# Kernel tuning notes

Hardware: AMD Instinct MI355X
Metric: run time of the kernel (lower is better)

## Reference

```python
import jax, jax.numpy as jnp
import numpy as np

KH, KW, STRIDE, PAD = 3, 3, 1, 1
TREE_DEPTH = 3
NUM_LEAVES = 2 ** TREE_DEPTH  # 8
NUM_NODES = NUM_LEAVES - 1    # 7
OUT_CH, IN_CH = 256, 64
B, H, W = 16, 48, 48
PATCH_LEN = IN_CH * KH * KW   # 576

# Each of the 16 relaxed binary logic gates g_k(a,b) is affine in (1, a, b, a*b):
#   g_k(a,b) = c0 + c1*a + c2*b + c3*(a*b)
# Rows follow the standard difflogic gate ordering (gate 3 = pass-through a).
GATE_COEFF = np.array([
    [0.,  0.,  0.,  0.],   # 0: FALSE
    [0.,  0.,  0.,  1.],   # 1: a AND b
    [0.,  1.,  0., -1.],   # 2: a AND NOT b
    [0.,  1.,  0.,  0.],   # 3: a
    [0.,  0.,  1., -1.],   # 4: NOT a AND b
    [0.,  0.,  1.,  0.],   # 5: b
    [0.,  1.,  1., -2.],   # 6: a XOR b
    [0.,  1.,  1., -1.],   # 7: a OR b
    [1., -1., -1.,  1.],   # 8: NOT (a OR b)
    [1., -1., -1.,  2.],   # 9: NOT (a XOR b)
    [1.,  0., -1.,  0.],   # 10: NOT b
    [1.,  0., -1.,  1.],   # 11: a OR NOT b
    [1., -1.,  0.,  0.],   # 12: NOT a
    [1., -1.,  0.,  1.],   # 13: NOT a OR b
    [1.,  0.,  0., -1.],   # 14: NOT (a AND b)
    [1.,  0.,  0.,  0.],   # 15: TRUE
], dtype=np.float32)


def _unfold(x):
    # x: (B, C, Hp, Wp) -> (B, C*KH*KW, Ho*Wo), channel-major then row-major
    # kernel ordering (matches torch.nn.functional.unfold).
    b, c, hp, wp = x.shape
    ho = (hp - KH) // STRIDE + 1
    wo = (wp - KW) // STRIDE + 1
    cols = jnp.stack(
        [x[:, :, i:i + STRIDE * ho:STRIDE, j:j + STRIDE * wo:STRIDE]
         for i in range(KH) for j in range(KW)], axis=2)  # (B, C, KH*KW, Ho, Wo)
    return cols.reshape(b, c * KH * KW, ho * wo), ho, wo


def setup_inputs() -> dict:
    key = jax.random.key(0)
    k1, k2, k3 = jax.random.split(key, 3)
    x = jax.random.uniform(k1, (B, IN_CH, H, W), dtype=jnp.float32)
    logits = jax.random.normal(k2, (OUT_CH, NUM_NODES, 16), dtype=jnp.float32)
    leaf_indices = jax.random.randint(k3, (OUT_CH, NUM_LEAVES), 0, PATCH_LEN, dtype=jnp.int32)
    return {"x": x, "logits": logits, "leaf_indices": leaf_indices}


def reference(x, logits, leaf_indices):
    b = x.shape[0]
    o = logits.shape[0]
    xp = jnp.pad(x, ((0, 0), (0, 0), (PAD, PAD), (PAD, PAD)))
    patches, ho, wo = _unfold(xp)          # (B, patch_len, L)
    cur = patches[:, leaf_indices, :]      # gather leaves: (B, O, num_leaves, L)
    coeff = jnp.asarray(GATE_COEFF)        # (16, 4)
    node_ptr = 0
    width = NUM_LEAVES
    for _ in range(TREE_DEPTH):
        nc = width // 2
        a = cur[:, :, 0::2, :]             # (B, O, nc, L)
        bb = cur[:, :, 1::2, :]
        probs = jax.nn.softmax(logits[:, node_ptr:node_ptr + nc, :], axis=-1)  # (O, nc, 16)
        # softmax-weighted mixture of the 16 gates = affine combo in (1, a, b, ab)
        w = jnp.einsum('ong,gc->onc', probs, coeff)  # (O, nc, 4)
        w = w[None, :, :, :, None]                   # (1, O, nc, 4, 1)
        cur = w[:, :, :, 0] + w[:, :, :, 1] * a + w[:, :, :, 2] * bb + w[:, :, :, 3] * (a * bb)
        node_ptr += nc
        width = nc
    y = cur[:, :, 0, :]                    # (B, O, L)
    return y.reshape(b, o, ho, wo)
```

## Files before the change

### kernel.cpp

```cpp
#include <hip/hip_runtime.h>

#define NB 16
#define IN_CH 64
#define OUT_CH 256
#define NH 48
#define NW 48
#define NPIX (NH * NW)
#define ROW_STRIDE 52
#define CH_STRIDE (4 * ROW_STRIDE)
#define LDS_DW (IN_CH * CH_STRIDE)
#define NITEMS (IN_CH * 4 * 26)
#define META_F4 9

__constant__ float c_gate[16 * 4] = {
    0.f, 0.f, 0.f, 0.f,
    0.f, 0.f, 0.f, 1.f,
    0.f, 1.f, 0.f, -1.f,
    0.f, 1.f, 0.f, 0.f,
    0.f, 0.f, 1.f, -1.f,
    0.f, 0.f, 1.f, 0.f,
    0.f, 1.f, 1.f, -2.f,
    0.f, 1.f, 1.f, -1.f,
    1.f, -1.f, -1.f, 1.f,
    1.f, -1.f, -1.f, 2.f,
    1.f, 0.f, -1.f, 0.f,
    1.f, 0.f, -1.f, 1.f,
    1.f, -1.f, 0.f, 0.f,
    1.f, -1.f, 0.f, 1.f,
    1.f, 0.f, 0.f, -1.f,
    1.f, 0.f, 0.f, 0.f
};

__global__ __launch_bounds__(256) void prep_kernel(
    const float* __restrict__ logits,
    const int*   __restrict__ leaf_idx,
    float*       __restrict__ meta)
{
    int t = blockIdx.x * 256 + threadIdx.x;
    if (t < OUT_CH * 8) {
        int idx = leaf_idx[t];
        int c  = idx / 9;
        int k  = idx - c * 9;
        int di = k / 3;
        int dj = k - di * 3;
        reinterpret_cast<int*>(meta)[(t >> 3) * 36 + (t & 7)] =
            c * CH_STRIDE + di * ROW_STRIDE + dj;
    } else {
        int t2 = t - OUT_CH * 8;
        if (t2 >= OUT_CH * 7) return;
        int o = t2 / 7;
        int n = t2 - o * 7;
        const float* lg = logits + (size_t)t2 * 16;

        float m = lg[0];
#pragma unroll
        for (int g = 1; g < 16; ++g) m = fmaxf(m, lg[g]);
        float e16[16];
        float s = 0.f;
#pragma unroll
        for (int g = 0; g < 16; ++g) { e16[g] = expf(lg[g] - m); s += e16[g]; }
        float inv = 1.f / s;

        float w0 = 0.f, w1 = 0.f, w2 = 0.f, w3 = 0.f;
#pragma unroll
        for (int g = 0; g < 16; ++g) {
            float p = e16[g] * inv;
            w0 += p * c_gate[g * 4 + 0];
            w1 += p * c_gate[g * 4 + 1];
            w2 += p * c_gate[g * 4 + 2];
            w3 += p * c_gate[g * 4 + 3];
        }
        float* mw = meta + o * 36 + 8 + n * 4;
        mw[0] = w0; mw[1] = w1; mw[2] = w2; mw[3] = w3;
    }
}

__global__ __launch_bounds__(512, 3) void ltc_kernel(
    const float*  __restrict__ x,
    const float4* __restrict__ meta,
    float*        __restrict__ out)
{
    __shared__ float lds[LDS_DW];

    const int band  = blockIdx.x;
    const int ohalf = blockIdx.y;
    const int b     = blockIdx.z;
    const int r0    = band * 2;
    const int tid   = threadIdx.x;

    const float* xb = x + (size_t)b * IN_CH * NPIX;
    for (int it = tid; it < NITEMS; it += 512) {
        int c   = it / 104;
        int rem = it - c * 104;
        int r4  = rem / 26;
        int p   = rem - r4 * 26;
        int gr  = r0 - 1 + r4;
        float2 v = make_float2(0.f, 0.f);
        if (p > 0 && p < 25 && (unsigned)gr < NH)
            v = *reinterpret_cast<const float2*>(xb + (c * NH + gr) * NW + (2 * p - 2));
        *reinterpret_cast<float2*>(&lds[c * CH_STRIDE + r4 * ROW_STRIDE + 2 * p]) = v;
    }
    __syncthreads();

    const int lane = tid & 63;
    const int wid  = tid >> 6;
    const int og   = lane >> 5;
    const int pxg  = lane & 31;
    const int o0   = ohalf * 128 + ((wid << 1) | og) * 8;

    int bases[3], opx[3];
#pragma unroll
    for (int g = 0; g < 3; ++g) {
        int px = g * 32 + pxg;
        int rr = (px >= 48) ? 1 : 0;
        int cc = px - rr * 48;
        bases[g] = rr * ROW_STRIDE + cc + 1;
        opx[g]   = (r0 + rr) * NW + cc;
    }

    const float4* mptr  = meta + (size_t)o0 * META_F4;
    float*        pbase = out + ((size_t)b * OUT_CH + o0) * NPIX;

    float4 F0 = mptr[0], F1 = mptr[1];

#pragma unroll 1
    for (int i = 0; i < 8; ++i) {
        float4 N0 = mptr[META_F4 + 0];
        float4 N1 = mptr[META_F4 + 1];

        float4 W0 = mptr[2], W1 = mptr[3], W2 = mptr[4];
        float4 W3 = mptr[5], W4 = mptr[6], W5 = mptr[7], W6 = mptr[8];

        const int off0 = __float_as_int(F0.x);
        const int off1 = __float_as_int(F0.y);
        const int off2 = __float_as_int(F0.z);
        const int off3 = __float_as_int(F0.w);
        const int off4 = __float_as_int(F1.x);
        const int off5 = __float_as_int(F1.y);
        const int off6 = __float_as_int(F1.z);
        const int off7 = __float_as_int(F1.w);

#pragma unroll
        for (int g = 0; g < 3; ++g) {
            const int bg = bases[g];
            float v0 = lds[off0 + bg];
            float v1 = lds[off1 + bg];
            float v2 = lds[off2 + bg];
            float v3 = lds[off3 + bg];
            float v4 = lds[off4 + bg];
            float v5 = lds[off5 + bg];
            float v6 = lds[off6 + bg];
            float v7 = lds[off7 + bg];
            float t0 = fmaf(v1, fmaf(W0.w, v0, W0.z), fmaf(W0.y, v0, W0.x));
            float t1 = fmaf(v3, fmaf(W1.w, v2, W1.z), fmaf(W1.y, v2, W1.x));
            float t2 = fmaf(v5, fmaf(W2.w, v4, W2.z), fmaf(W2.y, v4, W2.x));
            float t3 = fmaf(v7, fmaf(W3.w, v6, W3.z), fmaf(W3.y, v6, W3.x));
            float u0 = fmaf(t1, fmaf(W4.w, t0, W4.z), fmaf(W4.y, t0, W4.x));
            float u1 = fmaf(t3, fmaf(W5.w, t2, W5.z), fmaf(W5.y, t2, W5.x));
            float y  = fmaf(u1, fmaf(W6.w, u0, W6.z), fmaf(W6.y, u0, W6.x));
            pbase[opx[g]] = y;
        }

        F0 = N0; F1 = N1;
        mptr  += META_F4;
        pbase += NPIX;
    }
}

extern "C" void kernel_launch(void* const* d_in, const int* in_sizes, int n_in,
                              void* d_out, int out_size, void* d_ws, size_t ws_size,
                              hipStream_t stream) {
    const float* x        = (const float*)d_in[0];
    const float* logits   = (const float*)d_in[1];
    const int*   leaf_idx = (const int*)d_in[2];
    float*       out      = (float*)d_out;
    float*       meta     = (float*)d_ws;

    prep_kernel<<<15, 256, 0, stream>>>(logits, leaf_idx, meta);

    dim3 grid(24, 2, NB);
    ltc_kernel<<<grid, 512, 0, stream>>>(x, (const float4*)meta, out);
}
```

Measured before the change: 33.85 us.

## Retile to 4-row bands and 64 output channels per block

```diff
diff --git a/kernel.cpp b/kernel.cpp
--- a/kernel.cpp
+++ b/kernel.cpp
@@ -7,9 +7,10 @@
 #define NW 48
 #define NPIX (NH * NW)
 #define ROW_STRIDE 52
-#define CH_STRIDE (4 * ROW_STRIDE)
+#define HALO_ROWS 6
+#define CH_STRIDE (HALO_ROWS * ROW_STRIDE)
 #define LDS_DW (IN_CH * CH_STRIDE)
-#define NITEMS (IN_CH * 4 * 26)
+#define NITEMS (IN_CH * HALO_ROWS * 26)
 #define META_F4 9
 
 __constant__ float c_gate[16 * 4] = {
@@ -75,30 +76,45 @@
     }
 }
 
-__global__ __launch_bounds__(512, 3) void ltc_kernel(
+__device__ __forceinline__ float tree8(
+    const float v0, const float v1, const float v2, const float v3,
+    const float v4, const float v5, const float v6, const float v7,
+    const float4& W0, const float4& W1, const float4& W2, const float4& W3,
+    const float4& W4, const float4& W5, const float4& W6)
+{
+    float t0 = fmaf(v1, fmaf(W0.w, v0, W0.z), fmaf(W0.y, v0, W0.x));
+    float t1 = fmaf(v3, fmaf(W1.w, v2, W1.z), fmaf(W1.y, v2, W1.x));
+    float t2 = fmaf(v5, fmaf(W2.w, v4, W2.z), fmaf(W2.y, v4, W2.x));
+    float t3 = fmaf(v7, fmaf(W3.w, v6, W3.z), fmaf(W3.y, v6, W3.x));
+    float u0 = fmaf(t1, fmaf(W4.w, t0, W4.z), fmaf(W4.y, t0, W4.x));
+    float u1 = fmaf(t3, fmaf(W5.w, t2, W5.z), fmaf(W5.y, t2, W5.x));
+    return fmaf(u1, fmaf(W6.w, u0, W6.z), fmaf(W6.y, u0, W6.x));
+}
+
+__global__ __launch_bounds__(512, 4) void ltc_kernel(
     const float*  __restrict__ x,
     const float4* __restrict__ meta,
     float*        __restrict__ out)
 {
     __shared__ float lds[LDS_DW];
 
-    const int band  = blockIdx.x;
-    const int ohalf = blockIdx.y;
-    const int b     = blockIdx.z;
-    const int r0    = band * 2;
-    const int tid   = threadIdx.x;
+    const int band = blockIdx.x;
+    const int oq   = blockIdx.y;
+    const int b    = blockIdx.z;
+    const int r0   = band * 4;
+    const int tid  = threadIdx.x;
 
     const float* xb = x + (size_t)b * IN_CH * NPIX;
     for (int it = tid; it < NITEMS; it += 512) {
-        int c   = it / 104;
-        int rem = it - c * 104;
-        int r4  = rem / 26;
-        int p   = rem - r4 * 26;
-        int gr  = r0 - 1 + r4;
+        int c   = it / 156;
+        int rem = it - c * 156;
+        int r6  = rem / 26;
+        int p   = rem - r6 * 26;
+        int gr  = r0 - 1 + r6;
         float2 v = make_float2(0.f, 0.f);
         if (p > 0 && p < 25 && (unsigned)gr < NH)
             v = *reinterpret_cast<const float2*>(xb + (c * NH + gr) * NW + (2 * p - 2));
-        *reinterpret_cast<float2*>(&lds[c * CH_STRIDE + r4 * ROW_STRIDE + 2 * p]) = v;
+        *reinterpret_cast<float2*>(&lds[c * CH_STRIDE + r6 * ROW_STRIDE + 2 * p]) = v;
     }
     __syncthreads();
 
@@ -106,62 +122,54 @@
     const int wid  = tid >> 6;
     const int og   = lane >> 5;
     const int pxg  = lane & 31;
-    const int o0   = ohalf * 128 + ((wid << 1) | og) * 8;
+    const int o0   = oq * 64 + ((wid << 1) | og) * 4;
 
-    int bases[3], opx[3];
+    int bases[3];
 #pragma unroll
     for (int g = 0; g < 3; ++g) {
         int px = g * 32 + pxg;
         int rr = (px >= 48) ? 1 : 0;
         int cc = px - rr * 48;
         bases[g] = rr * ROW_STRIDE + cc + 1;
-        opx[g]   = (r0 + rr) * NW + cc;
     }
 
     const float4* mptr  = meta + (size_t)o0 * META_F4;
-    float*        pbase = out + ((size_t)b * OUT_CH + o0) * NPIX;
-
-    float4 F0 = mptr[0], F1 = mptr[1];
+    float*        pbase = out + ((size_t)b * OUT_CH + o0) * NPIX + r0 * NW + pxg;
 
 #pragma unroll 1
-    for (int i = 0; i < 8; ++i) {
-        float4 N0 = mptr[META_F4 + 0];
-        float4 N1 = mptr[META_F4 + 1];
-
+    for (int i = 0; i < 4; ++i) {
+        float4 M0 = mptr[0], M1 = mptr[1];
         float4 W0 = mptr[2], W1 = mptr[3], W2 = mptr[4];
         float4 W3 = mptr[5], W4 = mptr[6], W5 = mptr[7], W6 = mptr[8];
 
-        const int off0 = __float_as_int(F0.x);
-        const int off1 = __float_as_int(F0.y);
-        const int off2 = __float_as_int(F0.z);
-        const int off3 = __float_as_int(F0.w);
-        const int off4 = __float_as_int(F1.x);
-        const int off5 = __float_as_int(F1.y);
-        const int off6 = __float_as_int(F1.z);
-        const int off7 = __float_as_int(F1.w);
+        int off[8];
+        off[0] = __float_as_int(M0.x);
+        off[1] = __float_as_int(M0.y);
+        off[2] = __float_as_int(M0.z);
+        off[3] = __float_as_int(M0.w);
+        off[4] = __float_as_int(M1.x);
+        off[5] = __float_as_int(M1.y);
+        off[6] = __float_as_int(M1.z);
+        off[7] = __float_as_int(M1.w);
 
 #pragma unroll
         for (int g = 0; g < 3; ++g) {
             const int bg = bases[g];
-            float v0 = lds[off0 + bg];
-            float v1 = lds[off1 + bg];
-            float v2 = lds[off2 + bg];
-            float v3 = lds[off3 + bg];
-            float v4 = lds[off4 + bg];
-            float v5 = lds[off5 + bg];
-            float v6 = lds[off6 + bg];
-            float v7 = lds[off7 + bg];
-            float t0 = fmaf(v1, fmaf(W0.w, v0, W0.z), fmaf(W0.y, v0, W0.x));
-            float t1 = fmaf(v3, fmaf(W1.w, v2, W1.z), fmaf(W1.y, v2, W1.x));
-            float t2 = fmaf(v5, fmaf(W2.w, v4, W2.z), fmaf(W2.y, v4, W2.x));
-            float t3 = fmaf(v7, fmaf(W3.w, v6, W3.z), fmaf(W3.y, v6, W3.x));
-            float u0 = fmaf(t1, fmaf(W4.w, t0, W4.z), fmaf(W4.y, t0, W4.x));
-            float u1 = fmaf(t3, fmaf(W5.w, t2, W5.z), fmaf(W5.y, t2, W5.x));
-            float y  = fmaf(u1, fmaf(W6.w, u0, W6.z), fmaf(W6.y, u0, W6.x));
-            pbase[opx[g]] = y;
+            float a0[8], a1[8];
+#pragma unroll
+            for (int j = 0; j < 8; ++j) {
+                const int ad = off[j] + bg;
+                a0[j] = lds[ad];
+                a1[j] = lds[ad + 104];
+            }
+            float yA = tree8(a0[0],a0[1],a0[2],a0[3],a0[4],a0[5],a0[6],a0[7],
+                             W0,W1,W2,W3,W4,W5,W6);
+            float yB = tree8(a1[0],a1[1],a1[2],a1[3],a1[4],a1[5],a1[6],a1[7],
+                             W0,W1,W2,W3,W4,W5,W6);
+            pbase[g * 32]      = yA;
+            pbase[g * 32 + 96] = yB;
         }
 
-        F0 = N0; F1 = N1;
         mptr  += META_F4;
         pbase += NPIX;
     }
@@ -178,6 +186,6 @@
 
     prep_kernel<<<15, 256, 0, stream>>>(logits, leaf_idx, meta);
 
-    dim3 grid(24, 2, NB);
+    dim3 grid(12, 4, NB);
     ltc_kernel<<<grid, 512, 0, stream>>>(x, (const float4*)meta, out);
 }
```

Measured after the change: 69.21 us. 104% more time.
